# Kernel optimization log

Measured on AMD Instinct MI355X. Metric: run time of the kernel, lower is better.

The kernel has to match this reference:

```python
import jax, jax.numpy as jnp
import numpy as np

N, E, C, NB = 10000, 160000, 32, 8  # atoms, edges, channels, radial basis


def _W(k, shp):
    return jax.random.normal(k, shp, jnp.float32) / np.float32(np.sqrt(shp[0]))


def setup_inputs():
    ks = jax.random.split(jax.random.key(0), 16)
    return {
        "p1": jax.random.normal(ks[0], (N, C), jnp.float32),
        "p3": jax.random.normal(ks[1], (N, 3, C), jnp.float32),
        "r3": jax.random.normal(ks[2], (E, 3), jnp.float32),
        "basis": jax.random.normal(ks[3], (E, NB), jnp.float32),
        "idx_i": jax.random.randint(ks[4], (E,), 0, N, jnp.int32),
        "idx_j": jax.random.randint(ks[5], (E,), 0, N, jnp.int32),
        "pp1_W": _W(ks[6], (C, C)), "pp1_b": jnp.zeros((C,), jnp.float32),
        "pi1_W1": _W(ks[7], (2 * C, C)), "pi1_b1": jnp.zeros((C,), jnp.float32),
        "pi1_W2": _W(ks[8], (C, 3 * C)), "pi1_b2": jnp.zeros((3 * C,), jnp.float32),
        "pi1_W3": _W(ks[9], (3 * C, 3 * C * NB)),
        "ii1_W": _W(ks[10], (C, C)), "ii1_b": jnp.zeros((C,), jnp.float32),
        "pp3_W": _W(ks[11], (C, C)), "pp3_b": jnp.zeros((C,), jnp.float32),
        "pi3_W1": _W(ks[12], (2 * C, C)), "pi3_b1": jnp.zeros((C,), jnp.float32),
        "pi3_W2": _W(ks[13], (C, C)), "pi3_b2": jnp.zeros((C,), jnp.float32),
        "pi3_W3": _W(ks[14], (C, C * NB)),
        "ii3_W": _W(ks[15], (C, C)), "ii3_b": jnp.zeros((C,), jnp.float32),
    }


def _pi_layer(prop, idx_i, idx_j, basis, W1, b1, W2, b2, W3, out_c):
    # gather both endpoints, concat, linear MLP (no activation, no last bias),
    # contract trailing basis axis with per-edge basis functions
    inter = jnp.concatenate([prop[idx_i], prop[idx_j]], axis=-1)  # [E, ..., 2C]
    h = inter @ W1 + b1
    h = h @ W2 + b2
    h = h @ W3                                   # [E, ..., out_c*NB]
    h = h.reshape(h.shape[:-1] + (out_c, NB))
    return jnp.einsum('e...cb,eb->e...c', h, basis)


def _forward(p1, p3, r3, basis, idx_i, idx_j,
             pp1_W, pp1_b, pi1_W1, pi1_b1, pi1_W2, pi1_b2, pi1_W3, ii1_W, ii1_b,
             pp3_W, pp3_b, pi3_W1, pi3_b1, pi3_W2, pi3_b2, pi3_W3, ii3_W, ii3_b):
    act = jnp.tanh
    # rank-1 branch
    p1h = act(p1 @ pp1_W + pp1_b)                                   # [N, C]
    i1 = _pi_layer(p1h, idx_i, idx_j, basis,
                   pi1_W1, pi1_b1, pi1_W2, pi1_b2, pi1_W3, 3 * C)   # [E, 3C]
    i1_1, i1_2, i1_3 = jnp.split(i1, 3, axis=-1)
    i1a = act(i1_1 @ ii1_W + ii1_b)                                  # [E, C]
    p1n = jax.ops.segment_sum(i1a, idx_j, num_segments=N)            # [N, C]
    # rank-3 (vector) branch
    p3h = act(p3 @ pp3_W + pp3_b)                                    # [N, 3, C]
    i3 = _pi_layer(p3h, idx_i, idx_j, basis,
                   pi3_W1, pi3_b1, pi3_W2, pi3_b2, pi3_W3, C)        # [E, 3, C]
    i3 = act(i3 @ ii3_W + ii3_b)
    # equivariant scale/add: i3*i1_2 + r3*i1_3 (broadcast over Cartesian axis)
    i3 = i3 * i1_2[:, None, :] + r3[:, :, None] * i1_3[:, None, :]   # [E, 3, C]
    p3n = jax.ops.segment_sum(i3, idx_j, num_segments=N)             # [N, 3, C]
    # dot layer + residual into p1, then rescale p3 by p1
    p1o = jnp.sum(p3n * p3n, axis=1) + p1n                           # [N, C]
    p3o = p3n * p1o[:, None, :]                                      # [N, 3, C]
    return p1o, p3o


def reference(p1, p3, r3, basis, idx_i, idx_j,
              pp1_W, pp1_b, pi1_W1, pi1_b1, pi1_W2, pi1_b2, pi1_W3, ii1_W, ii1_b,
              pp3_W, pp3_b, pi3_W1, pi3_b1, pi3_W2, pi3_b2, pi3_W3, ii3_W, ii3_b):
    return _forward(p1, p3, r3, basis, idx_i, idx_j,
                    pp1_W, pp1_b, pi1_W1, pi1_b1, pi1_W2, pi1_b2, pi1_W3, ii1_W, ii1_b,
                    pp3_W, pp3_b, pi3_W1, pi3_b1, pi3_W2, pi3_b2, pi3_W3, ii3_W, ii3_b)
```

## Files before the change

kernel.cpp:

```cpp
#include <hip/hip_runtime.h>
#include <math.h>

#define NN 10000
#define NE 160000

typedef __attribute__((ext_vector_type(8))) short s8v;
typedef __attribute__((ext_vector_type(4))) float f4v;
typedef unsigned short u16;

#define OFF_P1HB 0u
#define OFF_P3HB 640000u
#define OFF_WB   2560000u
#define OFF_P1N  2764800u
#define OFF_P3N  4044800u

#define OW1T1 0
#define OW2T1 2304
#define OII1T 6144
#define OW1T3 7424
#define OW2T3 9728
#define OII3T 11008
#define OBLG  12288
#define OBL3G 92160
#define NWB   102400

__device__ __forceinline__ short f2b(float f) {
    unsigned u = __float_as_uint(f);
    u += 0x7fffu + ((u >> 16) & 1u);
    return (short)(u >> 16);
}
__device__ __forceinline__ float tanhf_fast(float x) {
    float xc = fminf(9.f, fmaxf(-9.f, x));
    float e = __expf(2.f * xc);
    return (e - 1.f) * __builtin_amdgcn_rcpf(e + 1.f);
}

__global__ __launch_bounds__(256) void node_prep(
    const float* __restrict__ p1, const float* __restrict__ p3,
    const float* __restrict__ pp1_W, const float* __restrict__ pp1_b,
    const float* __restrict__ pp3_W, const float* __restrict__ pp3_b,
    u16* __restrict__ p1hb, u16* __restrict__ p3hb)
{
    __shared__ float Ws[2][32 * 32];
    __shared__ float bsm[2][32];
    int tid = threadIdx.x;
    for (int i = tid; i < 32 * 32; i += 256) { Ws[0][i] = pp1_W[i]; Ws[1][i] = pp3_W[i]; }
    if (tid < 32) { bsm[0][tid] = pp1_b[tid]; bsm[1][tid] = pp3_b[tid]; }
    __syncthreads();
    int idx = blockIdx.x * 256 + tid;
    int n = idx >> 7;
    int r = (idx >> 5) & 3;
    int c = idx & 31;
    int sel = (r == 0) ? 0 : 1;
    const float* in = (r == 0) ? (p1 + n * 32) : (p3 + (n * 3 + (r - 1)) * 32);
    float acc = bsm[sel][c];
    #pragma unroll
    for (int k = 0; k < 32; ++k) acc += in[k] * Ws[sel][k * 32 + c];
    short v = f2b(tanhf(acc));
    if (r == 0) p1hb[n * 32 + c] = (u16)v;
    else        p3hb[(n * 3 + (r - 1)) * 32 + c] = (u16)v;
}

__global__ __launch_bounds__(256) void wprep(
    const float* __restrict__ W1, const float* __restrict__ W2,
    const float* __restrict__ W3, const float* __restrict__ ii1,
    const float* __restrict__ W13, const float* __restrict__ W23,
    const float* __restrict__ W33, const float* __restrict__ ii3,
    u16* __restrict__ wb)
{
    int i0 = blockIdx.x * 256 + threadIdx.x;
    if (i0 >= NWB) return;
    int i = i0;
    float v = 0.f;
    if (i < 2304) { int c = i / 72, k = i % 72; if (k < 64) v = W1[k * 32 + c]; }
    else if ((i -= 2304) < 3840) { int c = i / 40, k = i % 40; if (k < 32) v = W2[k * 96 + c]; }
    else if ((i -= 3840) < 1280) { int c = i / 40, k = i % 40; if (k < 32) v = ii1[k * 32 + c]; }
    else if ((i -= 1280) < 2304) { int c = i / 72, k = i % 72; if (k < 64) v = W13[k * 32 + c]; }
    else if ((i -= 2304) < 1280) { int c = i / 40, k = i % 40; if (k < 32) v = W23[k * 32 + c]; }
    else if ((i -= 1280) < 1280) { int c = i / 40, k = i % 40; if (k < 32) v = ii3[k * 32 + c]; }
    else if ((i -= 1280) < 79872) {
        int b = i / 9984, r = i % 9984, c = r / 104, k = r % 104;
        if (k < 96) v = W3[k * 768 + c * 8 + b];
    } else {
        i -= 79872;
        int b = i / 1280, r = i % 1280, c = r / 40, k = r % 40;
        if (k < 32) v = W33[k * 256 + c * 8 + b];
    }
    wb[i0] = (u16)f2b(v);
}

__global__ __launch_bounds__(64, 3) void edge_kernel(
    const u16* __restrict__ p1hb, const u16* __restrict__ p3hb,
    const float* __restrict__ r3, const float* __restrict__ basis,
    const int* __restrict__ idx_i, const int* __restrict__ idx_j,
    const u16* __restrict__ wb,
    const float* __restrict__ b1, const float* __restrict__ b2,
    const float* __restrict__ ii1b,
    const float* __restrict__ b13, const float* __restrict__ b23,
    const float* __restrict__ ii3b,
    float* __restrict__ p1n, float* __restrict__ p3n)
{
    __shared__ int4 smem4[400];
    char* sw = (char*)smem4;
    int*   sIdxI = (int*)(sw + 0);
    int*   sIdxJ = (int*)(sw + 128);
    float* sBasT = (float*)(sw + 256);
    float* sR3   = (float*)(sw + 1280);
    u16*   sT1   = (u16*)(sw + 1664);
    u16*   sT2   = (u16*)(sw + 4992);

    const int l   = threadIdx.x & 63;
    const int r16 = l & 15;
    const int kg  = l >> 4;
    const int ebase = blockIdx.x * 32;

    if (l < 32) sIdxI[l] = idx_i[ebase + l];
    else        sIdxJ[l - 32] = idx_j[ebase + l - 32];
    {
        int e = l & 31, hf = l >> 5;
        const float4* bp = (const float4*)(basis + (size_t)(ebase + e) * 8);
        float4 q = bp[hf];
        sBasT[(4 * hf + 0) * 32 + e] = q.x;
        sBasT[(4 * hf + 1) * 32 + e] = q.y;
        sBasT[(4 * hf + 2) * 32 + e] = q.z;
        sBasT[(4 * hf + 3) * 32 + e] = q.w;
        if (hf == 0) {
            sR3[e]      = r3[(size_t)(ebase + e) * 3 + 0];
            sR3[32 + e] = r3[(size_t)(ebase + e) * 3 + 1];
            sR3[64 + e] = r3[(size_t)(ebase + e) * 3 + 2];
        }
    }

    const float vb1[2]  = { b1[r16],   b1[16 + r16] };
    float vb2[6];
    #pragma unroll
    for (int nt = 0; nt < 6; ++nt) vb2[nt] = b2[16 * nt + r16];
    const float vii1[2] = { ii1b[r16], ii1b[16 + r16] };
    const float vb13[2] = { b13[r16],  b13[16 + r16] };
    const float vb23[2] = { b23[r16],  b23[16 + r16] };
    const float vii3[2] = { ii3b[r16], ii3b[16 + r16] };

    const f4v zf = {0.f, 0.f, 0.f, 0.f};

    s8v af[2][3];
    f4v accT[2][6];
    #pragma unroll
    for (int m = 0; m < 2; ++m)
        #pragma unroll
        for (int nt = 0; nt < 6; ++nt) accT[m][nt] = zf;

    const u16* gW1 = wb + OW1T1;
    const u16* gW2 = wb + OW2T1;
    #pragma unroll
    for (int m = 0; m < 2; ++m) {
        int rowA = m * 16 + r16;
        int ni = sIdxI[rowA], nj = sIdxJ[rowA];
        s8v av0 = *(const s8v*)(p1hb + (size_t)ni * 32 + kg * 8);
        s8v av1 = *(const s8v*)(p1hb + (size_t)nj * 32 + kg * 8);
        #pragma unroll
        for (int nt = 0; nt < 2; ++nt) {
            s8v bv0 = *(const s8v*)(gW1 + (16 * nt + r16) * 72 + 8 * kg);
            s8v bv1 = *(const s8v*)(gW1 + (16 * nt + r16) * 72 + 32 + 8 * kg);
            f4v a = __builtin_amdgcn_mfma_f32_16x16x32_bf16(av0, bv0, zf, 0, 0, 0);
            a = __builtin_amdgcn_mfma_f32_16x16x32_bf16(av1, bv1, a, 0, 0, 0);
            #pragma unroll
            for (int rr = 0; rr < 4; ++rr)
                sT2[(4 * kg + rr) * 40 + 16 * nt + r16] = (u16)f2b(a[rr] + vb1[nt]);
        }
        s8v av2 = *(const s8v*)(sT2 + r16 * 40 + 8 * kg);
        #pragma unroll
        for (int nt = 0; nt < 6; ++nt) {
            s8v bv = *(const s8v*)(gW2 + (16 * nt + r16) * 40 + 8 * kg);
            f4v acc = __builtin_amdgcn_mfma_f32_16x16x32_bf16(av2, bv, zf, 0, 0, 0);
            #pragma unroll
            for (int rr = 0; rr < 4; ++rr)
                sT1[(4 * kg + rr) * 104 + 16 * nt + r16] = (u16)f2b(acc[rr] + vb2[nt]);
        }
        af[m][0] = *(const s8v*)(sT1 + r16 * 104 + 8 * kg);
        af[m][1] = *(const s8v*)(sT1 + r16 * 104 + 32 + 8 * kg);
        af[m][2] = *(const s8v*)(sT1 + r16 * 104 + 64 + 8 * kg);
    }

    {
        const u16* gBl = wb + OBLG;
        #pragma unroll 2
        for (int b = 0; b < 8; ++b) {
            float tb[2][4];
            #pragma unroll
            for (int m = 0; m < 2; ++m)
                #pragma unroll
                for (int rr = 0; rr < 4; ++rr)
                    tb[m][rr] = sBasT[b * 32 + m * 16 + 4 * kg + rr];
            #pragma unroll
            for (int nt = 0; nt < 6; ++nt) {
                const u16* bp = gBl + (size_t)b * 9984 + (16 * nt + r16) * 104 + 8 * kg;
                s8v bv0 = *(const s8v*)(bp);
                s8v bv1 = *(const s8v*)(bp + 32);
                s8v bv2 = *(const s8v*)(bp + 64);
                #pragma unroll
                for (int m = 0; m < 2; ++m) {
                    f4v D = __builtin_amdgcn_mfma_f32_16x16x32_bf16(af[m][0], bv0, zf, 0, 0, 0);
                    D = __builtin_amdgcn_mfma_f32_16x16x32_bf16(af[m][1], bv1, D, 0, 0, 0);
                    D = __builtin_amdgcn_mfma_f32_16x16x32_bf16(af[m][2], bv2, D, 0, 0, 0);
                    #pragma unroll
                    for (int rr = 0; rr < 4; ++rr)
                        accT[m][nt][rr] += tb[m][rr] * D[rr];
                }
            }
        }
    }

    {
        const u16* gII = wb + OII1T;
        #pragma unroll
        for (int m = 0; m < 2; ++m) {
            #pragma unroll
            for (int nt = 0; nt < 2; ++nt)
                #pragma unroll
                for (int rr = 0; rr < 4; ++rr)
                    sT2[(4 * kg + rr) * 40 + 16 * nt + r16] = (u16)f2b(accT[m][nt][rr]);
            s8v av = *(const s8v*)(sT2 + r16 * 40 + 8 * kg);
            #pragma unroll
            for (int nt = 0; nt < 2; ++nt) {
                s8v bv = *(const s8v*)(gII + (16 * nt + r16) * 40 + 8 * kg);
                f4v ia = __builtin_amdgcn_mfma_f32_16x16x32_bf16(av, bv, zf, 0, 0, 0);
                #pragma unroll
                for (int rr = 0; rr < 4; ++rr) {
                    int rowD = m * 16 + 4 * kg + rr;
                    atomicAdd(&p1n[(size_t)sIdxJ[rowD] * 32 + 16 * nt + r16],
                              tanhf_fast(ia[rr] + vii1[nt]));
                }
            }
        }
    }

    const u16* gW13 = wb + OW1T3;
    const u16* gW23 = wb + OW2T3;
    const u16* gII3 = wb + OII3T;
    const u16* gBl3 = wb + OBL3G;
    for (int d = 0; d < 3; ++d) {
        s8v avG2[2];
        #pragma unroll
        for (int m = 0; m < 2; ++m) {
            int rowA = m * 16 + r16;
            int ni = sIdxI[rowA], nj = sIdxJ[rowA];
            s8v av0 = *(const s8v*)(p3hb + ((size_t)ni * 3 + d) * 32 + kg * 8);
            s8v av1 = *(const s8v*)(p3hb + ((size_t)nj * 3 + d) * 32 + kg * 8);
            #pragma unroll
            for (int nt = 0; nt < 2; ++nt) {
                s8v bv0 = *(const s8v*)(gW13 + (16 * nt + r16) * 72 + 8 * kg);
                s8v bv1 = *(const s8v*)(gW13 + (16 * nt + r16) * 72 + 32 + 8 * kg);
                f4v g = __builtin_amdgcn_mfma_f32_16x16x32_bf16(av0, bv0, zf, 0, 0, 0);
                g = __builtin_amdgcn_mfma_f32_16x16x32_bf16(av1, bv1, g, 0, 0, 0);
                #pragma unroll
                for (int rr = 0; rr < 4; ++rr)
                    sT2[(4 * kg + rr) * 40 + 16 * nt + r16] = (u16)f2b(g[rr] + vb13[nt]);
            }
            s8v avg = *(const s8v*)(sT2 + r16 * 40 + 8 * kg);
            #pragma unroll
            for (int nt = 0; nt < 2; ++nt) {
                s8v bv = *(const s8v*)(gW23 + (16 * nt + r16) * 40 + 8 * kg);
                f4v g2 = __builtin_amdgcn_mfma_f32_16x16x32_bf16(avg, bv, zf, 0, 0, 0);
                #pragma unroll
                for (int rr = 0; rr < 4; ++rr)
                    sT2[(4 * kg + rr) * 40 + 16 * nt + r16] = (u16)f2b(g2[rr] + vb23[nt]);
            }
            avG2[m] = *(const s8v*)(sT2 + r16 * 40 + 8 * kg);
        }
        f4v accP[2][2];
        #pragma unroll
        for (int m = 0; m < 2; ++m) { accP[m][0] = zf; accP[m][1] = zf; }
        #pragma unroll 2
        for (int b = 0; b < 8; ++b) {
            float tb[2][4];
            #pragma unroll
            for (int m = 0; m < 2; ++m)
                #pragma unroll
                for (int rr = 0; rr < 4; ++rr)
                    tb[m][rr] = sBasT[b * 32 + m * 16 + 4 * kg + rr];
            #pragma unroll
            for (int nt = 0; nt < 2; ++nt) {
                s8v bv = *(const s8v*)(gBl3 + (size_t)b * 1280 + (16 * nt + r16) * 40 + 8 * kg);
                #pragma unroll
                for (int m = 0; m < 2; ++m) {
                    f4v D = __builtin_amdgcn_mfma_f32_16x16x32_bf16(avG2[m], bv, zf, 0, 0, 0);
                    #pragma unroll
                    for (int rr = 0; rr < 4; ++rr)
                        accP[m][nt][rr] += tb[m][rr] * D[rr];
                }
            }
        }
        #pragma unroll
        for (int m = 0; m < 2; ++m) {
            #pragma unroll
            for (int nt = 0; nt < 2; ++nt)
                #pragma unroll
                for (int rr = 0; rr < 4; ++rr)
                    sT2[(4 * kg + rr) * 40 + 16 * nt + r16] = (u16)f2b(accP[m][nt][rr]);
            s8v av = *(const s8v*)(sT2 + r16 * 40 + 8 * kg);
            #pragma unroll
            for (int nt = 0; nt < 2; ++nt) {
                s8v bv = *(const s8v*)(gII3 + (16 * nt + r16) * 40 + 8 * kg);
                f4v ja = __builtin_amdgcn_mfma_f32_16x16x32_bf16(av, bv, zf, 0, 0, 0);
                #pragma unroll
                for (int rr = 0; rr < 4; ++rr) {
                    int rowD = m * 16 + 4 * kg + rr;
                    float i3a = tanhf_fast(ja[rr] + vii3[nt]);
                    float val = i3a * accT[m][2 + nt][rr] + sR3[d * 32 + rowD] * accT[m][4 + nt][rr];
                    atomicAdd(&p3n[((size_t)sIdxJ[rowD] * 3 + d) * 32 + 16 * nt + r16], val);
                }
            }
        }
    }
}

__global__ __launch_bounds__(256) void finalize_kernel(
    const float* __restrict__ p1n, const float* __restrict__ p3n,
    float* __restrict__ out)
{
    int t = blockIdx.x * 256 + threadIdx.x;
    int n = t >> 5, c = t & 31;
    float a0 = p3n[(n * 3 + 0) * 32 + c];
    float a1 = p3n[(n * 3 + 1) * 32 + c];
    float a2 = p3n[(n * 3 + 2) * 32 + c];
    float p1o = p1n[t] + a0 * a0 + a1 * a1 + a2 * a2;
    out[t] = p1o;
    float* o3 = out + NN * 32;
    o3[(n * 3 + 0) * 32 + c] = a0 * p1o;
    o3[(n * 3 + 1) * 32 + c] = a1 * p1o;
    o3[(n * 3 + 2) * 32 + c] = a2 * p1o;
}

extern "C" void kernel_launch(void* const* d_in, const int* in_sizes, int n_in,
                              void* d_out, int out_size, void* d_ws, size_t ws_size,
                              hipStream_t stream) {
    const float* p1     = (const float*)d_in[0];
    const float* p3     = (const float*)d_in[1];
    const float* r3     = (const float*)d_in[2];
    const float* basis  = (const float*)d_in[3];
    const int*   idx_i  = (const int*)d_in[4];
    const int*   idx_j  = (const int*)d_in[5];
    const float* pp1_W  = (const float*)d_in[6];
    const float* pp1_b  = (const float*)d_in[7];
    const float* pi1_W1 = (const float*)d_in[8];
    const float* pi1_b1 = (const float*)d_in[9];
    const float* pi1_W2 = (const float*)d_in[10];
    const float* pi1_b2 = (const float*)d_in[11];
    const float* pi1_W3 = (const float*)d_in[12];
    const float* ii1_W  = (const float*)d_in[13];
    const float* ii1_b  = (const float*)d_in[14];
    const float* pp3_W  = (const float*)d_in[15];
    const float* pp3_b  = (const float*)d_in[16];
    const float* pi3_W1 = (const float*)d_in[17];
    const float* pi3_b1 = (const float*)d_in[18];
    const float* pi3_W2 = (const float*)d_in[19];
    const float* pi3_b2 = (const float*)d_in[20];
    const float* pi3_W3 = (const float*)d_in[21];
    const float* ii3_W  = (const float*)d_in[22];
    const float* ii3_b  = (const float*)d_in[23];

    char* ws = (char*)d_ws;
    u16*   p1hb = (u16*)(ws + OFF_P1HB);
    u16*   p3hb = (u16*)(ws + OFF_P3HB);
    u16*   wb   = (u16*)(ws + OFF_WB);
    float* p1n  = (float*)(ws + OFF_P1N);
    float* p3n  = (float*)(ws + OFF_P3N);

    hipMemsetAsync(p1n, 0, 5120000, stream);

    node_prep<<<dim3(5000), dim3(256), 0, stream>>>(p1, p3, pp1_W, pp1_b, pp3_W, pp3_b, p1hb, p3hb);
    wprep<<<dim3((NWB + 255) / 256), dim3(256), 0, stream>>>(
        pi1_W1, pi1_W2, pi1_W3, ii1_W, pi3_W1, pi3_W2, pi3_W3, ii3_W, wb);

    edge_kernel<<<dim3(NE / 32), dim3(64), 0, stream>>>(
        p1hb, p3hb, r3, basis, idx_i, idx_j, wb,
        pi1_b1, pi1_b2, ii1_b, pi3_b1, pi3_b2, ii3_b,
        p1n, p3n);

    finalize_kernel<<<dim3(1250), dim3(256), 0, stream>>>(p1n, p3n, (float*)d_out);
}
```

Before: 134.7 us.

## Stage basis-weight tiles in LDS shared by four waves with fragment-ordered weight layout

Weights are now pre-laid-out in MFMA fragment order, so each lane reads one contiguous 16-byte chunk and the padding is gone. The edge kernel moves from one wave to four waves per block, 128 edges per block. The large per-basis W3 slices and the W33 block are staged cooperatively into LDS, with register prefetch of the next slice, so the four waves share each global read. This removes redundant global/L2 weight traffic per wave. In exchange it adds block-wide barriers and about 43 KB of LDS per block, which may reduce occupancy.

```diff
diff --git a/kernel.cpp b/kernel.cpp
--- a/kernel.cpp
+++ b/kernel.cpp
@@ -15,14 +15,14 @@
 #define OFF_P3N  4044800u
 
 #define OW1T1 0
-#define OW2T1 2304
-#define OII1T 6144
-#define OW1T3 7424
-#define OW2T3 9728
-#define OII3T 11008
-#define OBLG  12288
-#define OBL3G 92160
-#define NWB   102400
+#define OW2T1 2048
+#define OII1T 5120
+#define OW1T3 6144
+#define OW2T3 8192
+#define OII3T 9216
+#define OBLG  10240
+#define OBL3G 83968
+#define NWB   92160
 
 __device__ __forceinline__ short f2b(float f) {
     unsigned u = __float_as_uint(f);
@@ -71,25 +71,42 @@
     int i0 = blockIdx.x * 256 + threadIdx.x;
     if (i0 >= NWB) return;
     int i = i0;
-    float v = 0.f;
-    if (i < 2304) { int c = i / 72, k = i % 72; if (k < 64) v = W1[k * 32 + c]; }
-    else if ((i -= 2304) < 3840) { int c = i / 40, k = i % 40; if (k < 32) v = W2[k * 96 + c]; }
-    else if ((i -= 3840) < 1280) { int c = i / 40, k = i % 40; if (k < 32) v = ii1[k * 32 + c]; }
-    else if ((i -= 1280) < 2304) { int c = i / 72, k = i % 72; if (k < 64) v = W13[k * 32 + c]; }
-    else if ((i -= 2304) < 1280) { int c = i / 40, k = i % 40; if (k < 32) v = W23[k * 32 + c]; }
-    else if ((i -= 1280) < 1280) { int c = i / 40, k = i % 40; if (k < 32) v = ii3[k * 32 + c]; }
-    else if ((i -= 1280) < 79872) {
-        int b = i / 9984, r = i % 9984, c = r / 104, k = r % 104;
-        if (k < 96) v = W3[k * 768 + c * 8 + b];
+    float v;
+    if (i < 2048) {
+        int j = i & 7, L = (i >> 3) & 63, ks = (i >> 9) & 1, nt = i >> 10;
+        v = W1[(ks * 32 + (L >> 4) * 8 + j) * 32 + 16 * nt + (L & 15)];
+    } else if ((i -= 2048) < 3072) {
+        int j = i & 7, L = (i >> 3) & 63, nt = i >> 9;
+        v = W2[((L >> 4) * 8 + j) * 96 + 16 * nt + (L & 15)];
+    } else if ((i -= 3072) < 1024) {
+        int j = i & 7, L = (i >> 3) & 63, nt = i >> 9;
+        v = ii1[((L >> 4) * 8 + j) * 32 + 16 * nt + (L & 15)];
+    } else if ((i -= 1024) < 2048) {
+        int j = i & 7, L = (i >> 3) & 63, ks = (i >> 9) & 1, nt = i >> 10;
+        v = W13[(ks * 32 + (L >> 4) * 8 + j) * 32 + 16 * nt + (L & 15)];
+    } else if ((i -= 2048) < 1024) {
+        int j = i & 7, L = (i >> 3) & 63, nt = i >> 9;
+        v = W23[((L >> 4) * 8 + j) * 32 + 16 * nt + (L & 15)];
+    } else if ((i -= 1024) < 1024) {
+        int j = i & 7, L = (i >> 3) & 63, nt = i >> 9;
+        v = ii3[((L >> 4) * 8 + j) * 32 + 16 * nt + (L & 15)];
+    } else if ((i -= 1024) < 73728) {
+        int b = i / 9216, r = i % 9216;
+        int nt = r / 1536, r2 = r % 1536;
+        int ks = r2 / 512, r3 = r2 & 511;
+        int L = r3 >> 3, j = r3 & 7;
+        v = W3[(ks * 32 + (L >> 4) * 8 + j) * 768 + (16 * nt + (L & 15)) * 8 + b];
     } else {
-        i -= 79872;
-        int b = i / 1280, r = i % 1280, c = r / 40, k = r % 40;
-        if (k < 32) v = W33[k * 256 + c * 8 + b];
+        i -= 73728;
+        int b = i >> 10, r = i & 1023;
+        int nt = r >> 9, r3 = r & 511;
+        int L = r3 >> 3, j = r3 & 7;
+        v = W33[((L >> 4) * 8 + j) * 256 + (16 * nt + (L & 15)) * 8 + b];
     }
     wb[i0] = (u16)f2b(v);
 }
 
-__global__ __launch_bounds__(64, 3) void edge_kernel(
+__global__ __launch_bounds__(256, 3) void edge_kernel(
     const u16* __restrict__ p1hb, const u16* __restrict__ p3hb,
     const float* __restrict__ r3, const float* __restrict__ basis,
     const int* __restrict__ idx_i, const int* __restrict__ idx_j,
@@ -100,8 +117,10 @@
     const float* __restrict__ ii3b,
     float* __restrict__ p1n, float* __restrict__ p3n)
 {
-    __shared__ int4 smem4[400];
-    char* sw = (char*)smem4;
+    __shared__ int4 smem4[43520 / 16];
+    char* sm  = (char*)smem4;
+    u16*  sBl = (u16*)sm;
+    char* sw  = sm + 18432 + ((threadIdx.x >> 6) * 6272);
     int*   sIdxI = (int*)(sw + 0);
     int*   sIdxJ = (int*)(sw + 128);
     float* sBasT = (float*)(sw + 256);
@@ -109,17 +128,18 @@
     u16*   sT1   = (u16*)(sw + 1664);
     u16*   sT2   = (u16*)(sw + 4992);
 
-    const int l   = threadIdx.x & 63;
+    const int tid = threadIdx.x;
+    const int w   = tid >> 6;
+    const int l   = tid & 63;
     const int r16 = l & 15;
     const int kg  = l >> 4;
-    const int ebase = blockIdx.x * 32;
+    const int ebase = blockIdx.x * 128 + w * 32;
 
     if (l < 32) sIdxI[l] = idx_i[ebase + l];
     else        sIdxJ[l - 32] = idx_j[ebase + l - 32];
     {
         int e = l & 31, hf = l >> 5;
-        const float4* bp = (const float4*)(basis + (size_t)(ebase + e) * 8);
-        float4 q = bp[hf];
+        float4 q = ((const float4*)(basis + (size_t)(ebase + e) * 8))[hf];
         sBasT[(4 * hf + 0) * 32 + e] = q.x;
         sBasT[(4 * hf + 1) * 32 + e] = q.y;
         sBasT[(4 * hf + 2) * 32 + e] = q.z;
@@ -149,42 +169,63 @@
         #pragma unroll
         for (int nt = 0; nt < 6; ++nt) accT[m][nt] = zf;
 
-    const u16* gW1 = wb + OW1T1;
-    const u16* gW2 = wb + OW2T1;
-    #pragma unroll
-    for (int m = 0; m < 2; ++m) {
-        int rowA = m * 16 + r16;
-        int ni = sIdxI[rowA], nj = sIdxJ[rowA];
-        s8v av0 = *(const s8v*)(p1hb + (size_t)ni * 32 + kg * 8);
-        s8v av1 = *(const s8v*)(p1hb + (size_t)nj * 32 + kg * 8);
-        #pragma unroll
-        for (int nt = 0; nt < 2; ++nt) {
-            s8v bv0 = *(const s8v*)(gW1 + (16 * nt + r16) * 72 + 8 * kg);
-            s8v bv1 = *(const s8v*)(gW1 + (16 * nt + r16) * 72 + 32 + 8 * kg);
-            f4v a = __builtin_amdgcn_mfma_f32_16x16x32_bf16(av0, bv0, zf, 0, 0, 0);
-            a = __builtin_amdgcn_mfma_f32_16x16x32_bf16(av1, bv1, a, 0, 0, 0);
-            #pragma unroll
-            for (int rr = 0; rr < 4; ++rr)
-                sT2[(4 * kg + rr) * 40 + 16 * nt + r16] = (u16)f2b(a[rr] + vb1[nt]);
-        }
-        s8v av2 = *(const s8v*)(sT2 + r16 * 40 + 8 * kg);
-        #pragma unroll
-        for (int nt = 0; nt < 6; ++nt) {
-            s8v bv = *(const s8v*)(gW2 + (16 * nt + r16) * 40 + 8 * kg);
-            f4v acc = __builtin_amdgcn_mfma_f32_16x16x32_bf16(av2, bv, zf, 0, 0, 0);
-            #pragma unroll
-            for (int rr = 0; rr < 4; ++rr)
-                sT1[(4 * kg + rr) * 104 + 16 * nt + r16] = (u16)f2b(acc[rr] + vb2[nt]);
-        }
-        af[m][0] = *(const s8v*)(sT1 + r16 * 104 + 8 * kg);
-        af[m][1] = *(const s8v*)(sT1 + r16 * 104 + 32 + 8 * kg);
-        af[m][2] = *(const s8v*)(sT1 + r16 * 104 + 64 + 8 * kg);
-    }
-
     {
-        const u16* gBl = wb + OBLG;
-        #pragma unroll 2
+        const u16* gW1 = wb + OW1T1;
+        const u16* gW2 = wb + OW2T1;
+        #pragma unroll
+        for (int m = 0; m < 2; ++m) {
+            int rowA = m * 16 + r16;
+            int ni = sIdxI[rowA], nj = sIdxJ[rowA];
+            s8v av0 = *(const s8v*)(p1hb + (size_t)ni * 32 + kg * 8);
+            s8v av1 = *(const s8v*)(p1hb + (size_t)nj * 32 + kg * 8);
+            #pragma unroll
+            for (int nt = 0; nt < 2; ++nt) {
+                s8v bv0 = *(const s8v*)(gW1 + ((nt * 2 + 0) * 64 + l) * 8);
+                s8v bv1 = *(const s8v*)(gW1 + ((nt * 2 + 1) * 64 + l) * 8);
+                f4v a = __builtin_amdgcn_mfma_f32_16x16x32_bf16(av0, bv0, zf, 0, 0, 0);
+                a = __builtin_amdgcn_mfma_f32_16x16x32_bf16(av1, bv1, a, 0, 0, 0);
+                #pragma unroll
+                for (int rr = 0; rr < 4; ++rr)
+                    sT2[(4 * kg + rr) * 40 + 16 * nt + r16] = (u16)f2b(a[rr] + vb1[nt]);
+            }
+            s8v av2 = *(const s8v*)(sT2 + r16 * 40 + 8 * kg);
+            #pragma unroll
+            for (int nt = 0; nt < 6; ++nt) {
+                s8v bv = *(const s8v*)(gW2 + (nt * 64 + l) * 8);
+                f4v acc = __builtin_amdgcn_mfma_f32_16x16x32_bf16(av2, bv, zf, 0, 0, 0);
+                #pragma unroll
+                for (int rr = 0; rr < 4; ++rr)
+                    sT1[(4 * kg + rr) * 104 + 16 * nt + r16] = (u16)f2b(acc[rr] + vb2[nt]);
+            }
+            af[m][0] = *(const s8v*)(sT1 + r16 * 104 + 8 * kg);
+            af[m][1] = *(const s8v*)(sT1 + r16 * 104 + 32 + 8 * kg);
+            af[m][2] = *(const s8v*)(sT1 + r16 * 104 + 64 + 8 * kg);
+        }
+    }
+
+    {
+        const int4* gBl2 = (const int4*)(wb + OBLG);
+        int4 tmp[5];
+        #pragma unroll
+        for (int i = 0; i < 5; ++i) {
+            int r = w + 4 * i;
+            if (r < 18) tmp[i] = gBl2[r * 64 + l];
+        }
         for (int b = 0; b < 8; ++b) {
+            __syncthreads();
+            #pragma unroll
+            for (int i = 0; i < 5; ++i) {
+                int r = w + 4 * i;
+                if (r < 18) ((int4*)sBl)[r * 64 + l] = tmp[i];
+            }
+            __syncthreads();
+            if (b < 7) {
+                #pragma unroll
+                for (int i = 0; i < 5; ++i) {
+                    int r = w + 4 * i;
+                    if (r < 18) tmp[i] = gBl2[(size_t)(b + 1) * 1152 + r * 64 + l];
+                }
+            }
             float tb[2][4];
             #pragma unroll
             for (int m = 0; m < 2; ++m)
@@ -193,10 +234,9 @@
                     tb[m][rr] = sBasT[b * 32 + m * 16 + 4 * kg + rr];
             #pragma unroll
             for (int nt = 0; nt < 6; ++nt) {
-                const u16* bp = gBl + (size_t)b * 9984 + (16 * nt + r16) * 104 + 8 * kg;
-                s8v bv0 = *(const s8v*)(bp);
-                s8v bv1 = *(const s8v*)(bp + 32);
-                s8v bv2 = *(const s8v*)(bp + 64);
+                s8v bv0 = *(const s8v*)(sBl + ((nt * 3 + 0) * 64 + l) * 8);
+                s8v bv1 = *(const s8v*)(sBl + ((nt * 3 + 1) * 64 + l) * 8);
+                s8v bv2 = *(const s8v*)(sBl + ((nt * 3 + 2) * 64 + l) * 8);
                 #pragma unroll
                 for (int m = 0; m < 2; ++m) {
                     f4v D = __builtin_amdgcn_mfma_f32_16x16x32_bf16(af[m][0], bv0, zf, 0, 0, 0);
@@ -222,7 +262,7 @@
             s8v av = *(const s8v*)(sT2 + r16 * 40 + 8 * kg);
             #pragma unroll
             for (int nt = 0; nt < 2; ++nt) {
-                s8v bv = *(const s8v*)(gII + (16 * nt + r16) * 40 + 8 * kg);
+                s8v bv = *(const s8v*)(gII + (nt * 64 + l) * 8);
                 f4v ia = __builtin_amdgcn_mfma_f32_16x16x32_bf16(av, bv, zf, 0, 0, 0);
                 #pragma unroll
                 for (int rr = 0; rr < 4; ++rr) {
@@ -234,10 +274,20 @@
         }
     }
 
+    {
+        const int4* gBl3v = (const int4*)(wb + OBL3G);
+        int4 t3[4];
+        #pragma unroll
+        for (int i = 0; i < 4; ++i) t3[i] = gBl3v[(w + 4 * i) * 64 + l];
+        __syncthreads();
+        #pragma unroll
+        for (int i = 0; i < 4; ++i) ((int4*)sBl)[(w + 4 * i) * 64 + l] = t3[i];
+        __syncthreads();
+    }
+
     const u16* gW13 = wb + OW1T3;
     const u16* gW23 = wb + OW2T3;
     const u16* gII3 = wb + OII3T;
-    const u16* gBl3 = wb + OBL3G;
     for (int d = 0; d < 3; ++d) {
         s8v avG2[2];
         #pragma unroll
@@ -248,8 +298,8 @@
             s8v av1 = *(const s8v*)(p3hb + ((size_t)nj * 3 + d) * 32 + kg * 8);
             #pragma unroll
             for (int nt = 0; nt < 2; ++nt) {
-                s8v bv0 = *(const s8v*)(gW13 + (16 * nt + r16) * 72 + 8 * kg);
-                s8v bv1 = *(const s8v*)(gW13 + (16 * nt + r16) * 72 + 32 + 8 * kg);
+                s8v bv0 = *(const s8v*)(gW13 + ((nt * 2 + 0) * 64 + l) * 8);
+                s8v bv1 = *(const s8v*)(gW13 + ((nt * 2 + 1) * 64 + l) * 8);
                 f4v g = __builtin_amdgcn_mfma_f32_16x16x32_bf16(av0, bv0, zf, 0, 0, 0);
                 g = __builtin_amdgcn_mfma_f32_16x16x32_bf16(av1, bv1, g, 0, 0, 0);
                 #pragma unroll
@@ -259,7 +309,7 @@
             s8v avg = *(const s8v*)(sT2 + r16 * 40 + 8 * kg);
             #pragma unroll
             for (int nt = 0; nt < 2; ++nt) {
-                s8v bv = *(const s8v*)(gW23 + (16 * nt + r16) * 40 + 8 * kg);
+                s8v bv = *(const s8v*)(gW23 + (nt * 64 + l) * 8);
                 f4v g2 = __builtin_amdgcn_mfma_f32_16x16x32_bf16(avg, bv, zf, 0, 0, 0);
                 #pragma unroll
                 for (int rr = 0; rr < 4; ++rr)
@@ -280,7 +330,7 @@
                     tb[m][rr] = sBasT[b * 32 + m * 16 + 4 * kg + rr];
             #pragma unroll
             for (int nt = 0; nt < 2; ++nt) {
-                s8v bv = *(const s8v*)(gBl3 + (size_t)b * 1280 + (16 * nt + r16) * 40 + 8 * kg);
+                s8v bv = *(const s8v*)(sBl + ((b * 2 + nt) * 64 + l) * 8);
                 #pragma unroll
                 for (int m = 0; m < 2; ++m) {
                     f4v D = __builtin_amdgcn_mfma_f32_16x16x32_bf16(avG2[m], bv, zf, 0, 0, 0);
@@ -300,7 +350,7 @@
             s8v av = *(const s8v*)(sT2 + r16 * 40 + 8 * kg);
             #pragma unroll
             for (int nt = 0; nt < 2; ++nt) {
-                s8v bv = *(const s8v*)(gII3 + (16 * nt + r16) * 40 + 8 * kg);
+                s8v bv = *(const s8v*)(gII3 + (nt * 64 + l) * 8);
                 f4v ja = __builtin_amdgcn_mfma_f32_16x16x32_bf16(av, bv, zf, 0, 0, 0);
                 #pragma unroll
                 for (int rr = 0; rr < 4; ++rr) {
@@ -369,10 +419,10 @@
     hipMemsetAsync(p1n, 0, 5120000, stream);
 
     node_prep<<<dim3(5000), dim3(256), 0, stream>>>(p1, p3, pp1_W, pp1_b, pp3_W, pp3_b, p1hb, p3hb);
-    wprep<<<dim3((NWB + 255) / 256), dim3(256), 0, stream>>>(
+    wprep<<<dim3(NWB / 256), dim3(256), 0, stream>>>(
         pi1_W1, pi1_W2, pi1_W3, ii1_W, pi3_W1, pi3_W2, pi3_W3, ii3_W, wb);
 
-    edge_kernel<<<dim3(NE / 32), dim3(64), 0, stream>>>(
+    edge_kernel<<<dim3(NE / 128), dim3(256), 0, stream>>>(
         p1hb, p3hb, r3, basis, idx_i, idx_j, wb,
         pi1_b1, pi1_b2, ii1_b, pi3_b1, pi3_b2, ii3_b,
         p1n, p3n);
```

Result: slower. 165.1 us (+22.6%).

## Fold linear MLP chain W1·W2·W3 into one precomputed per-basis weight

Applied to the files above, without the earlier changes.

Because the pi-layer MLP has no activations, the three weight matrices (and biases) are premultiplied in two small prep kernels into a single 64→C·NB matrix per basis, plus a bias term that is applied through an MFMA with the basis as A operand. The edge kernel then does one 2-MFMA contraction per tile instead of three chained GEMMs with shared-memory round trips and bf16 requantization of intermediates. Weights are also repacked into the MFMA fragment order for coalesced per-lane loads. It adds a launch and precompute work, and rounding the fused weights to bf16 changes numerics slightly.

```diff
diff --git a/kernel.cpp b/kernel.cpp
--- a/kernel.cpp
+++ b/kernel.cpp
@@ -11,18 +11,17 @@
 #define OFF_P1HB 0u
 #define OFF_P3HB 640000u
 #define OFF_WB   2560000u
-#define OFF_P1N  2764800u
-#define OFF_P3N  4044800u
-
-#define OW1T1 0
-#define OW2T1 2304
-#define OII1T 6144
-#define OW1T3 7424
-#define OW2T3 9728
-#define OII3T 11008
-#define OBLG  12288
-#define OBL3G 92160
-#define NWB   102400
+#define OFF_SCR  2703360u
+#define OFF_P1N  2736640u
+#define OFF_P3N  4016640u
+
+#define OWF1  0
+#define OBB1  49152
+#define OII1T 52224
+#define OWF3  53248
+#define OBB3  69632
+#define OII3T 70656
+#define NWB   71680
 
 __device__ __forceinline__ short f2b(float f) {
     unsigned u = __float_as_uint(f);
@@ -61,30 +60,107 @@
     else        p3hb[(n * 3 + (r - 1)) * 32 + c] = (u16)v;
 }
 
-__global__ __launch_bounds__(256) void wprep(
+__global__ __launch_bounds__(256) void wprep1(
     const float* __restrict__ W1, const float* __restrict__ W2,
-    const float* __restrict__ W3, const float* __restrict__ ii1,
+    const float* __restrict__ b1, const float* __restrict__ b2,
     const float* __restrict__ W13, const float* __restrict__ W23,
-    const float* __restrict__ W33, const float* __restrict__ ii3,
-    u16* __restrict__ wb)
+    const float* __restrict__ b13, const float* __restrict__ b23,
+    float* __restrict__ scr)
 {
+    float* T1  = scr;
+    float* T3  = scr + 6144;
+    float* bt1 = scr + 8192;
+    float* bt3 = scr + 8288;
+    int i = blockIdx.x * 256 + threadIdx.x;
+    if (i < 6144) {
+        int r = i / 96, c = i % 96;
+        float a = 0.f;
+        #pragma unroll 8
+        for (int k = 0; k < 32; ++k) a += W1[r * 32 + k] * W2[k * 96 + c];
+        T1[i] = a;
+    } else if ((i -= 6144) < 2048) {
+        int r = i / 32, c = i % 32;
+        float a = 0.f;
+        #pragma unroll 8
+        for (int k = 0; k < 32; ++k) a += W13[r * 32 + k] * W23[k * 32 + c];
+        T3[i] = a;
+    } else if ((i -= 2048) < 96) {
+        float a = b2[i];
+        #pragma unroll 8
+        for (int k = 0; k < 32; ++k) a += b1[k] * W2[k * 96 + i];
+        bt1[i] = a;
+    } else if ((i -= 96) < 32) {
+        float a = b23[i];
+        #pragma unroll 8
+        for (int k = 0; k < 32; ++k) a += b13[k] * W23[k * 32 + i];
+        bt3[i] = a;
+    }
+}
+
+__global__ __launch_bounds__(256) void wprep2(
+    const float* __restrict__ W3, const float* __restrict__ W33,
+    const float* __restrict__ ii1, const float* __restrict__ ii3,
+    const float* __restrict__ scr, u16* __restrict__ wb)
+{
+    const float* T1  = scr;
+    const float* T3  = scr + 6144;
+    const float* bt1 = scr + 8192;
+    const float* bt3 = scr + 8288;
     int i0 = blockIdx.x * 256 + threadIdx.x;
     if (i0 >= NWB) return;
     int i = i0;
     float v = 0.f;
-    if (i < 2304) { int c = i / 72, k = i % 72; if (k < 64) v = W1[k * 32 + c]; }
-    else if ((i -= 2304) < 3840) { int c = i / 40, k = i % 40; if (k < 32) v = W2[k * 96 + c]; }
-    else if ((i -= 3840) < 1280) { int c = i / 40, k = i % 40; if (k < 32) v = ii1[k * 32 + c]; }
-    else if ((i -= 1280) < 2304) { int c = i / 72, k = i % 72; if (k < 64) v = W13[k * 32 + c]; }
-    else if ((i -= 2304) < 1280) { int c = i / 40, k = i % 40; if (k < 32) v = W23[k * 32 + c]; }
-    else if ((i -= 1280) < 1280) { int c = i / 40, k = i % 40; if (k < 32) v = ii3[k * 32 + c]; }
-    else if ((i -= 1280) < 79872) {
-        int b = i / 9984, r = i % 9984, c = r / 104, k = r % 104;
-        if (k < 96) v = W3[k * 768 + c * 8 + b];
+    if (i < 49152) {
+        int b = i / 6144, r = i % 6144;
+        int nt = r / 1024, r2 = r % 1024;
+        int ks = r2 / 512, r3 = r2 & 511;
+        int L = r3 >> 3, j = r3 & 7;
+        int k = ks * 32 + (L >> 4) * 8 + j;
+        int c = 16 * nt + (L & 15);
+        float a = 0.f;
+        #pragma unroll 8
+        for (int q = 0; q < 96; ++q) a += T1[k * 96 + q] * W3[q * 768 + c * 8 + b];
+        v = a;
+    } else if ((i -= 49152) < 3072) {
+        int nt = i / 512, r3 = i & 511;
+        int L = r3 >> 3, j = r3 & 7;
+        if ((L >> 4) == 0) {
+            int x = (16 * nt + (L & 15)) * 8 + j;
+            float a = 0.f;
+            #pragma unroll 8
+            for (int q = 0; q < 96; ++q) a += bt1[q] * W3[q * 768 + x];
+            v = a;
+        }
+    } else if ((i -= 3072) < 1024) {
+        int nt = i / 512, r3 = i & 511;
+        int L = r3 >> 3, j = r3 & 7;
+        v = ii1[((L >> 4) * 8 + j) * 32 + 16 * nt + (L & 15)];
+    } else if ((i -= 1024) < 16384) {
+        int b = i / 2048, r = i % 2048;
+        int nt = r / 1024, r2 = r % 1024;
+        int ks = r2 / 512, r3 = r2 & 511;
+        int L = r3 >> 3, j = r3 & 7;
+        int k = ks * 32 + (L >> 4) * 8 + j;
+        int c = 16 * nt + (L & 15);
+        float a = 0.f;
+        #pragma unroll 8
+        for (int q = 0; q < 32; ++q) a += T3[k * 32 + q] * W33[q * 256 + c * 8 + b];
+        v = a;
+    } else if ((i -= 16384) < 1024) {
+        int nt = i / 512, r3 = i & 511;
+        int L = r3 >> 3, j = r3 & 7;
+        if ((L >> 4) == 0) {
+            int x = (16 * nt + (L & 15)) * 8 + j;
+            float a = 0.f;
+            #pragma unroll 8
+            for (int q = 0; q < 32; ++q) a += bt3[q] * W33[q * 256 + x];
+            v = a;
+        }
     } else {
-        i -= 79872;
-        int b = i / 1280, r = i % 1280, c = r / 40, k = r % 40;
-        if (k < 32) v = W33[k * 256 + c * 8 + b];
+        i -= 1024;
+        int nt = i / 512, r3 = i & 511;
+        int L = r3 >> 3, j = r3 & 7;
+        v = ii3[((L >> 4) * 8 + j) * 32 + 16 * nt + (L & 15)];
     }
     wb[i0] = (u16)f2b(v);
 }
@@ -94,20 +170,16 @@
     const float* __restrict__ r3, const float* __restrict__ basis,
     const int* __restrict__ idx_i, const int* __restrict__ idx_j,
     const u16* __restrict__ wb,
-    const float* __restrict__ b1, const float* __restrict__ b2,
-    const float* __restrict__ ii1b,
-    const float* __restrict__ b13, const float* __restrict__ b23,
-    const float* __restrict__ ii3b,
+    const float* __restrict__ ii1b, const float* __restrict__ ii3b,
     float* __restrict__ p1n, float* __restrict__ p3n)
 {
-    __shared__ int4 smem4[400];
+    __shared__ int4 smem4[192];
     char* sw = (char*)smem4;
     int*   sIdxI = (int*)(sw + 0);
     int*   sIdxJ = (int*)(sw + 128);
     float* sBasT = (float*)(sw + 256);
     float* sR3   = (float*)(sw + 1280);
-    u16*   sT1   = (u16*)(sw + 1664);
-    u16*   sT2   = (u16*)(sw + 4992);
+    u16*   sT2   = (u16*)(sw + 1664);
 
     const int l   = threadIdx.x & 63;
     const int r16 = l & 15;
@@ -131,58 +203,43 @@
         }
     }
 
-    const float vb1[2]  = { b1[r16],   b1[16 + r16] };
-    float vb2[6];
+    const float vii1[2] = { ii1b[r16], ii1b[16 + r16] };
+    const float vii3[2] = { ii3b[r16], ii3b[16 + r16] };
+
+    const f4v zf = {0.f, 0.f, 0.f, 0.f};
+
+    s8v bA[2];
     #pragma unroll
-    for (int nt = 0; nt < 6; ++nt) vb2[nt] = b2[16 * nt + r16];
-    const float vii1[2] = { ii1b[r16], ii1b[16 + r16] };
-    const float vb13[2] = { b13[r16],  b13[16 + r16] };
-    const float vb23[2] = { b23[r16],  b23[16 + r16] };
-    const float vii3[2] = { ii3b[r16], ii3b[16 + r16] };
-
-    const f4v zf = {0.f, 0.f, 0.f, 0.f};
-
-    s8v af[2][3];
-    f4v accT[2][6];
-    #pragma unroll
-    for (int m = 0; m < 2; ++m)
-        #pragma unroll
-        for (int nt = 0; nt < 6; ++nt) accT[m][nt] = zf;
-
-    const u16* gW1 = wb + OW1T1;
-    const u16* gW2 = wb + OW2T1;
+    for (int m = 0; m < 2; ++m) {
+        s8v t;
+        #pragma unroll
+        for (int j = 0; j < 8; ++j)
+            t[j] = (kg == 0) ? f2b(sBasT[j * 32 + m * 16 + r16]) : (short)0;
+        bA[m] = t;
+    }
+
+    s8v avI[2], avJ[2];
     #pragma unroll
     for (int m = 0; m < 2; ++m) {
         int rowA = m * 16 + r16;
-        int ni = sIdxI[rowA], nj = sIdxJ[rowA];
-        s8v av0 = *(const s8v*)(p1hb + (size_t)ni * 32 + kg * 8);
-        s8v av1 = *(const s8v*)(p1hb + (size_t)nj * 32 + kg * 8);
-        #pragma unroll
-        for (int nt = 0; nt < 2; ++nt) {
-            s8v bv0 = *(const s8v*)(gW1 + (16 * nt + r16) * 72 + 8 * kg);
-            s8v bv1 = *(const s8v*)(gW1 + (16 * nt + r16) * 72 + 32 + 8 * kg);
-            f4v a = __builtin_amdgcn_mfma_f32_16x16x32_bf16(av0, bv0, zf, 0, 0, 0);
-            a = __builtin_amdgcn_mfma_f32_16x16x32_bf16(av1, bv1, a, 0, 0, 0);
-            #pragma unroll
-            for (int rr = 0; rr < 4; ++rr)
-                sT2[(4 * kg + rr) * 40 + 16 * nt + r16] = (u16)f2b(a[rr] + vb1[nt]);
-        }
-        s8v av2 = *(const s8v*)(sT2 + r16 * 40 + 8 * kg);
+        avI[m] = *(const s8v*)(p1hb + (size_t)sIdxI[rowA] * 32 + kg * 8);
+        avJ[m] = *(const s8v*)(p1hb + (size_t)sIdxJ[rowA] * 32 + kg * 8);
+    }
+
+    f4v accT[2][6];
+    {
+        const u16* gBB = wb + OBB1;
         #pragma unroll
         for (int nt = 0; nt < 6; ++nt) {
-            s8v bv = *(const s8v*)(gW2 + (16 * nt + r16) * 40 + 8 * kg);
-            f4v acc = __builtin_amdgcn_mfma_f32_16x16x32_bf16(av2, bv, zf, 0, 0, 0);
-            #pragma unroll
-            for (int rr = 0; rr < 4; ++rr)
-                sT1[(4 * kg + rr) * 104 + 16 * nt + r16] = (u16)f2b(acc[rr] + vb2[nt]);
-        }
-        af[m][0] = *(const s8v*)(sT1 + r16 * 104 + 8 * kg);
-        af[m][1] = *(const s8v*)(sT1 + r16 * 104 + 32 + 8 * kg);
-        af[m][2] = *(const s8v*)(sT1 + r16 * 104 + 64 + 8 * kg);
+            s8v bbv = *(const s8v*)(gBB + (nt * 64 + l) * 8);
+            #pragma unroll
+            for (int m = 0; m < 2; ++m)
+                accT[m][nt] = __builtin_amdgcn_mfma_f32_16x16x32_bf16(bA[m], bbv, zf, 0, 0, 0);
+        }
     }
 
     {
-        const u16* gBl = wb + OBLG;
+        const u16* gW = wb + OWF1;
         #pragma unroll 2
         for (int b = 0; b < 8; ++b) {
             float tb[2][4];
@@ -193,15 +250,13 @@
                     tb[m][rr] = sBasT[b * 32 + m * 16 + 4 * kg + rr];
             #pragma unroll
             for (int nt = 0; nt < 6; ++nt) {
-                const u16* bp = gBl + (size_t)b * 9984 + (16 * nt + r16) * 104 + 8 * kg;
+                const u16* bp = gW + ((size_t)(b * 6 + nt) * 2) * 512 + l * 8;
                 s8v bv0 = *(const s8v*)(bp);
-                s8v bv1 = *(const s8v*)(bp + 32);
-                s8v bv2 = *(const s8v*)(bp + 64);
+                s8v bv1 = *(const s8v*)(bp + 512);
                 #pragma unroll
                 for (int m = 0; m < 2; ++m) {
-                    f4v D = __builtin_amdgcn_mfma_f32_16x16x32_bf16(af[m][0], bv0, zf, 0, 0, 0);
-                    D = __builtin_amdgcn_mfma_f32_16x16x32_bf16(af[m][1], bv1, D, 0, 0, 0);
-                    D = __builtin_amdgcn_mfma_f32_16x16x32_bf16(af[m][2], bv2, D, 0, 0, 0);
+                    f4v D = __builtin_amdgcn_mfma_f32_16x16x32_bf16(avI[m], bv0, zf, 0, 0, 0);
+                    D = __builtin_amdgcn_mfma_f32_16x16x32_bf16(avJ[m], bv1, D, 0, 0, 0);
                     #pragma unroll
                     for (int rr = 0; rr < 4; ++rr)
                         accT[m][nt][rr] += tb[m][rr] * D[rr];
@@ -222,7 +277,7 @@
             s8v av = *(const s8v*)(sT2 + r16 * 40 + 8 * kg);
             #pragma unroll
             for (int nt = 0; nt < 2; ++nt) {
-                s8v bv = *(const s8v*)(gII + (16 * nt + r16) * 40 + 8 * kg);
+                s8v bv = *(const s8v*)(gII + (nt * 64 + l) * 8);
                 f4v ia = __builtin_amdgcn_mfma_f32_16x16x32_bf16(av, bv, zf, 0, 0, 0);
                 #pragma unroll
                 for (int rr = 0; rr < 4; ++rr) {
@@ -234,42 +289,25 @@
         }
     }
 
-    const u16* gW13 = wb + OW1T3;
-    const u16* gW23 = wb + OW2T3;
+    const u16* gW3  = wb + OWF3;
+    const u16* gBB3 = wb + OBB3;
     const u16* gII3 = wb + OII3T;
-    const u16* gBl3 = wb + OBL3G;
     for (int d = 0; d < 3; ++d) {
-        s8v avG2[2];
+        s8v avI3[2], avJ3[2];
         #pragma unroll
         for (int m = 0; m < 2; ++m) {
             int rowA = m * 16 + r16;
-            int ni = sIdxI[rowA], nj = sIdxJ[rowA];
-            s8v av0 = *(const s8v*)(p3hb + ((size_t)ni * 3 + d) * 32 + kg * 8);
-            s8v av1 = *(const s8v*)(p3hb + ((size_t)nj * 3 + d) * 32 + kg * 8);
-            #pragma unroll
-            for (int nt = 0; nt < 2; ++nt) {
-                s8v bv0 = *(const s8v*)(gW13 + (16 * nt + r16) * 72 + 8 * kg);
-                s8v bv1 = *(const s8v*)(gW13 + (16 * nt + r16) * 72 + 32 + 8 * kg);
-                f4v g = __builtin_amdgcn_mfma_f32_16x16x32_bf16(av0, bv0, zf, 0, 0, 0);
-                g = __builtin_amdgcn_mfma_f32_16x16x32_bf16(av1, bv1, g, 0, 0, 0);
-                #pragma unroll
-                for (int rr = 0; rr < 4; ++rr)
-                    sT2[(4 * kg + rr) * 40 + 16 * nt + r16] = (u16)f2b(g[rr] + vb13[nt]);
-            }
-            s8v avg = *(const s8v*)(sT2 + r16 * 40 + 8 * kg);
-            #pragma unroll
-            for (int nt = 0; nt < 2; ++nt) {
-                s8v bv = *(const s8v*)(gW23 + (16 * nt + r16) * 40 + 8 * kg);
-                f4v g2 = __builtin_amdgcn_mfma_f32_16x16x32_bf16(avg, bv, zf, 0, 0, 0);
-                #pragma unroll
-                for (int rr = 0; rr < 4; ++rr)
-                    sT2[(4 * kg + rr) * 40 + 16 * nt + r16] = (u16)f2b(g2[rr] + vb23[nt]);
-            }
-            avG2[m] = *(const s8v*)(sT2 + r16 * 40 + 8 * kg);
+            avI3[m] = *(const s8v*)(p3hb + ((size_t)sIdxI[rowA] * 3 + d) * 32 + kg * 8);
+            avJ3[m] = *(const s8v*)(p3hb + ((size_t)sIdxJ[rowA] * 3 + d) * 32 + kg * 8);
         }
         f4v accP[2][2];
         #pragma unroll
-        for (int m = 0; m < 2; ++m) { accP[m][0] = zf; accP[m][1] = zf; }
+        for (int nt = 0; nt < 2; ++nt) {
+            s8v bbv = *(const s8v*)(gBB3 + (nt * 64 + l) * 8);
+            #pragma unroll
+            for (int m = 0; m < 2; ++m)
+                accP[m][nt] = __builtin_amdgcn_mfma_f32_16x16x32_bf16(bA[m], bbv, zf, 0, 0, 0);
+        }
         #pragma unroll 2
         for (int b = 0; b < 8; ++b) {
             float tb[2][4];
@@ -280,10 +318,13 @@
                     tb[m][rr] = sBasT[b * 32 + m * 16 + 4 * kg + rr];
             #pragma unroll
             for (int nt = 0; nt < 2; ++nt) {
-                s8v bv = *(const s8v*)(gBl3 + (size_t)b * 1280 + (16 * nt + r16) * 40 + 8 * kg);
+                const u16* bp = gW3 + ((size_t)(b * 2 + nt) * 2) * 512 + l * 8;
+                s8v bv0 = *(const s8v*)(bp);
+                s8v bv1 = *(const s8v*)(bp + 512);
                 #pragma unroll
                 for (int m = 0; m < 2; ++m) {
-                    f4v D = __builtin_amdgcn_mfma_f32_16x16x32_bf16(avG2[m], bv, zf, 0, 0, 0);
+                    f4v D = __builtin_amdgcn_mfma_f32_16x16x32_bf16(avI3[m], bv0, zf, 0, 0, 0);
+                    D = __builtin_amdgcn_mfma_f32_16x16x32_bf16(avJ3[m], bv1, D, 0, 0, 0);
                     #pragma unroll
                     for (int rr = 0; rr < 4; ++rr)
                         accP[m][nt][rr] += tb[m][rr] * D[rr];
@@ -300,7 +341,7 @@
             s8v av = *(const s8v*)(sT2 + r16 * 40 + 8 * kg);
             #pragma unroll
             for (int nt = 0; nt < 2; ++nt) {
-                s8v bv = *(const s8v*)(gII3 + (16 * nt + r16) * 40 + 8 * kg);
+                s8v bv = *(const s8v*)(gII3 + (nt * 64 + l) * 8);
                 f4v ja = __builtin_amdgcn_mfma_f32_16x16x32_bf16(av, bv, zf, 0, 0, 0);
                 #pragma unroll
                 for (int rr = 0; rr < 4; ++rr) {
@@ -363,19 +404,21 @@
     u16*   p1hb = (u16*)(ws + OFF_P1HB);
     u16*   p3hb = (u16*)(ws + OFF_P3HB);
     u16*   wb   = (u16*)(ws + OFF_WB);
+    float* scr  = (float*)(ws + OFF_SCR);
     float* p1n  = (float*)(ws + OFF_P1N);
     float* p3n  = (float*)(ws + OFF_P3N);
 
     hipMemsetAsync(p1n, 0, 5120000, stream);
 
     node_prep<<<dim3(5000), dim3(256), 0, stream>>>(p1, p3, pp1_W, pp1_b, pp3_W, pp3_b, p1hb, p3hb);
-    wprep<<<dim3((NWB + 255) / 256), dim3(256), 0, stream>>>(
-        pi1_W1, pi1_W2, pi1_W3, ii1_W, pi3_W1, pi3_W2, pi3_W3, ii3_W, wb);
+    wprep1<<<dim3(33), dim3(256), 0, stream>>>(
+        pi1_W1, pi1_W2, pi1_b1, pi1_b2, pi3_W1, pi3_W2, pi3_b1, pi3_b2, scr);
+    wprep2<<<dim3(NWB / 256), dim3(256), 0, stream>>>(
+        pi1_W3, pi3_W3, ii1_W, ii3_W, scr, wb);
 
     edge_kernel<<<dim3(NE / 32), dim3(64), 0, stream>>>(
         p1hb, p3hb, r3, basis, idx_i, idx_j, wb,
-        pi1_b1, pi1_b2, ii1_b, pi3_b1, pi3_b2, ii3_b,
-        p1n, p3n);
+        ii1_b, ii3_b, p1n, p3n);
 
     finalize_kernel<<<dim3(1250), dim3(256), 0, stream>>>(p1n, p3n, (float*)d_out);
 }
```

Measured after the change: 136.9 us. No clear change (+1.7%).
